# Kernel tuning notes

Hardware: AMD Instinct MI355X
Metric: run time of the kernel (lower is better)

Reference implementation:

```python
import jax, jax.numpy as jnp
import numpy as np

N_AGENTS = 5
RNN = 128
ATT = 64
N_ACT = 10
IN_DIM = 256
SIZE = 65535  # multiple of N_AGENTS -> padding branch never taken
TAU = 0.01


def _gru_cell(x, h, w_ih, w_hh, b_ih, b_hh):
    # PyTorch GRUCell math
    gi = x @ w_ih.T + b_ih
    gh = h @ w_hh.T + b_hh
    i_r, i_z, i_n = jnp.split(gi, 3, axis=-1)
    h_r, h_z, h_n = jnp.split(gh, 3, axis=-1)
    r = jax.nn.sigmoid(i_r + h_r)
    z = jax.nn.sigmoid(i_z + h_z)
    n = jnp.tanh(i_n + r * h_n)
    return (1.0 - z) * n + z * h


def _gru_seq(xs, w_ih, w_hh, b_ih, b_hh):
    # xs: [T, B, D]; zero initial hidden, returns all step outputs [T, B, RNN]
    h0 = jnp.zeros((xs.shape[1], RNN), xs.dtype)
    def step(h, x):
        h2 = _gru_cell(x, h, w_ih, w_hh, b_ih, b_hh)
        return h2, h2
    _, ys = jax.lax.scan(step, h0, xs)
    return ys


def setup_inputs():
    key = jax.random.key(0)
    ks = jax.random.split(key, 26)
    def u(k, shape, fan):
        return jax.random.uniform(k, shape, jnp.float32, -1.0, 1.0) / np.sqrt(fan)
    return {
        'obs': jax.random.normal(ks[0], (SIZE, IN_DIM), jnp.float32),
        'hidden_state': jax.random.normal(ks[1], (SIZE, RNN), jnp.float32),
        'enc_w': u(ks[2], (RNN, IN_DIM), IN_DIM), 'enc_b': u(ks[3], (RNN,), IN_DIM),
        'gru_w_ih': u(ks[4], (3 * RNN, RNN), RNN), 'gru_w_hh': u(ks[5], (3 * RNN, RNN), RNN),
        'gru_b_ih': u(ks[6], (3 * RNN,), RNN), 'gru_b_hh': u(ks[7], (3 * RNN,), RNN),
        'bi_w_ih_f': u(ks[8], (3 * RNN, 2 * RNN), RNN), 'bi_w_hh_f': u(ks[9], (3 * RNN, RNN), RNN),
        'bi_b_ih_f': u(ks[10], (3 * RNN,), RNN), 'bi_b_hh_f': u(ks[11], (3 * RNN,), RNN),
        'bi_w_ih_r': u(ks[12], (3 * RNN, 2 * RNN), RNN), 'bi_w_hh_r': u(ks[13], (3 * RNN, RNN), RNN),
        'bi_b_ih_r': u(ks[14], (3 * RNN,), RNN), 'bi_b_hh_r': u(ks[15], (3 * RNN,), RNN),
        'hard_w': u(ks[16], (2, 2 * RNN), 2 * RNN), 'hard_b': u(ks[17], (2,), 2 * RNN),
        'q_w': u(ks[18], (ATT, RNN), RNN),
        'k_w': u(ks[19], (ATT, RNN), RNN),
        'v_w': u(ks[20], (ATT, RNN), RNN), 'v_b': u(ks[21], (ATT,), RNN),
        'dec_w': u(ks[22], (N_ACT, RNN + ATT), RNN + ATT), 'dec_b': u(ks[23], (N_ACT,), RNN + ATT),
    }


def reference(obs, hidden_state, enc_w, enc_b, gru_w_ih, gru_w_hh, gru_b_ih, gru_b_hh,
              bi_w_ih_f, bi_w_hh_f, bi_b_ih_f, bi_b_hh_f,
              bi_w_ih_r, bi_w_hh_r, bi_b_ih_r, bi_b_hh_r,
              hard_w, hard_b, q_w, k_w, v_w, v_b, dec_w, dec_b):
    size = obs.shape[0]
    bpa = size // N_AGENTS  # batch per agent; SIZE is a multiple of N_AGENTS

    x = jax.nn.relu(obs @ enc_w.T + enc_b)
    h_out = _gru_cell(x, hidden_state, gru_w_ih, gru_w_hh, gru_b_ih, gru_b_hh)

    # --- hard attention: pairwise agent features -> bi-GRU -> gumbel-softmax gate ---
    # (computed exactly as in the original; note the original soft_attention
    #  ignores hard_weights, so this does not influence the returned output)
    h = h_out.reshape(bpa, N_AGENTS, RNN)
    nbr = np.array([[j for j in range(N_AGENTS) if j != i] for i in range(N_AGENTS)])  # [n, n-1]
    h_i = jnp.broadcast_to(h[:, :, None, :], (bpa, N_AGENTS, N_AGENTS - 1, RNN))
    h_j = h[:, nbr, :]                              # [bpa, n, n-1, RNN]
    pair = jnp.concatenate([h_i, h_j], axis=-1)     # [bpa, n, n-1, 2*RNN]
    seq = pair.transpose(2, 0, 1, 3).reshape(N_AGENTS - 1, bpa * N_AGENTS, 2 * RNN)
    fwd = _gru_seq(seq, bi_w_ih_f, bi_w_hh_f, bi_b_ih_f, bi_b_hh_f)
    bwd = _gru_seq(seq[::-1], bi_w_ih_r, bi_w_hh_r, bi_b_ih_r, bi_b_hh_r)[::-1]
    h_hard = jnp.concatenate([fwd, bwd], axis=-1)   # [n-1, B, 2*RNN]
    h_hard = h_hard.transpose(1, 0, 2).reshape(-1, 2 * RNN)
    logits = h_hard @ hard_w.T + hard_b             # [B*(n-1), 2]
    u01 = jax.random.uniform(jax.random.key(42), logits.shape, jnp.float32, 1e-10, 1.0)
    gumbel = -jnp.log(-jnp.log(u01))
    gs = jax.nn.softmax((logits + gumbel) / TAU, axis=-1)
    hard_weights = gs[:, 1].reshape(bpa, N_AGENTS, 1, N_AGENTS - 1).transpose(1, 0, 2, 3)
    _ = hard_weights  # unused downstream, matching the original module

    # --- soft attention: original loops per sample doing a 1x1 matmul+softmax;
    #     vectorized here. softmax over a single element is identically 1. ---
    q = h_out @ q_w.T
    k = h_out @ k_w.T
    v = jax.nn.relu(h_out @ v_w.T + v_b)
    score = jnp.sum(q * k, axis=-1, keepdims=True) / np.sqrt(ATT)  # [B,1]
    soft_w = jax.nn.softmax(score, axis=-1)                         # all ones
    x_att = v * soft_w

    final_input = jnp.concatenate([h_out, x_att], axis=-1)
    output = final_input @ dec_w.T + dec_b
    return output, h_out
```

## Files before the change

### kernel.cpp

```cpp
#include <hip/hip_runtime.h>
#include <stdint.h>

#define SIZE 65535

typedef __bf16 bf16x8 __attribute__((ext_vector_type(8)));
typedef float floatx4 __attribute__((ext_vector_type(4)));

#define WS_ENCW 0
#define WS_WIH  32768
#define WS_WHH  81920
#define WS_VW   131072
#define WS_DECW 139264
#define WS_TOTC 17792

__device__ __forceinline__ unsigned short f2bf(float f) {
    union { float f; unsigned int u; } v; v.f = f;
    unsigned int u = v.u;
    return (unsigned short)((u + 0x7fffu + ((u >> 16) & 1u)) >> 16);
}
__device__ __forceinline__ float bf2f(unsigned short b) {
    union { unsigned int u; float f; } v; v.u = ((unsigned int)b) << 16;
    return v.f;
}
__device__ __forceinline__ float sigmf(float x) {
    x = fminf(fmaxf(x, -30.f), 30.f);
    return 1.f / (1.f + __expf(-x));
}
__device__ __forceinline__ float tanhfast(float x) {
    x = fminf(fmaxf(x, -15.f), 15.f);
    float e = __expf(2.f * x);
    return (e - 1.f) / (e + 1.f);
}

union BF8 { bf16x8 v; unsigned short s[8]; };

__device__ __forceinline__ bf16x8 cvt8g(const float* p) {
    float4 a = *reinterpret_cast<const float4*>(p);
    float4 b = *reinterpret_cast<const float4*>(p + 4);
    BF8 r;
    r.s[0] = f2bf(a.x); r.s[1] = f2bf(a.y); r.s[2] = f2bf(a.z); r.s[3] = f2bf(a.w);
    r.s[4] = f2bf(b.x); r.s[5] = f2bf(b.y); r.s[6] = f2bf(b.z); r.s[7] = f2bf(b.w);
    return r.v;
}
__device__ __forceinline__ bf16x8 ld8(const unsigned short* p) {
    return *reinterpret_cast<const bf16x8*>(p);
}

__global__ __launch_bounds__(256) void cvt_weights(
    const float* __restrict__ enc_w, const float* __restrict__ w_ih,
    const float* __restrict__ w_hh, const float* __restrict__ v_w,
    const float* __restrict__ dec_w, unsigned short* __restrict__ ws) {
    int c = blockIdx.x * 256 + threadIdx.x;
    if (c >= WS_TOTC) return;
    const int lane = c & 63;
    const int l = lane & 15;
    const int q = lane >> 4;
    const float* src; int row, col, stride; bool zero = false;
    if (c < 4096) {
        int lt = c >> 6; int nt = lt >> 3, kt = lt & 7;
        row = nt * 16 + l; col = kt * 32 + q * 8; src = enc_w; stride = 256;
    } else if (c < 10240) {
        int lt = (c - 4096) >> 6; int nt = lt / 12; int r2 = lt % 12;
        int g = r2 >> 2, kt = r2 & 3;
        row = g * 128 + nt * 16 + l; col = kt * 32 + q * 8; src = w_ih; stride = 128;
    } else if (c < 16384) {
        int lt = (c - 10240) >> 6; int nt = lt / 12; int r2 = lt % 12;
        int g = r2 >> 2, kt = r2 & 3;
        row = g * 128 + nt * 16 + l; col = kt * 32 + q * 8; src = w_hh; stride = 128;
    } else if (c < 17408) {
        int lt = (c - 16384) >> 6; int nt = lt >> 2, kt = lt & 3;
        row = nt * 16 + l; col = kt * 32 + q * 8; src = v_w; stride = 128;
    } else {
        int kt = (c - 17408) >> 6;
        row = l; col = kt * 32 + q * 8; src = dec_w; stride = 192;
        zero = (l >= 10);
    }
    float4 a, b;
    if (zero) { a = make_float4(0.f,0.f,0.f,0.f); b = a; }
    else {
        const float* p = src + (size_t)row * stride + col;
        a = *reinterpret_cast<const float4*>(p);
        b = *reinterpret_cast<const float4*>(p + 4);
    }
    unsigned short* d = ws + (size_t)c * 8;
    d[0]=f2bf(a.x); d[1]=f2bf(a.y); d[2]=f2bf(a.z); d[3]=f2bf(a.w);
    d[4]=f2bf(b.x); d[5]=f2bf(b.y); d[6]=f2bf(b.z); d[7]=f2bf(b.w);
}

__global__ __launch_bounds__(256, 4) void attn_critic_kernel(
    const float* __restrict__ obs,
    const float* __restrict__ hid,
    const float* __restrict__ enc_b,
    const float* __restrict__ b_ih,
    const float* __restrict__ b_hh,
    const float* __restrict__ v_b,
    const float* __restrict__ dec_b,
    const unsigned short* __restrict__ wsw,
    float* __restrict__ out)
{
    __shared__ __align__(16) unsigned short sA[4][16][136];
    __shared__ __align__(16) unsigned short sV[4][16][72];
    __shared__ __align__(16) float sO[4][16][10];

    const int tid  = threadIdx.x;
    const int wave = tid >> 6;
    const int lane = tid & 63;
    const int l15  = lane & 15;
    const int quad = lane >> 4;
    const int wrow0 = (blockIdx.x * 4 + wave) * 16;

    int rA0 = wrow0 + l15; rA0 = (rA0 < SIZE) ? rA0 : (SIZE - 1);

    bf16x8 aob[8], hf[4];
    {
        const float* o0 = obs + (size_t)rA0 * 256;
#pragma unroll
        for (int kt = 0; kt < 8; ++kt)
            aob[kt] = cvt8g(o0 + kt * 32 + quad * 8);
        const float* h0 = hid + (size_t)rA0 * 128;
#pragma unroll
        for (int kt = 0; kt < 4; ++kt)
            hf[kt] = cvt8g(h0 + kt * 32 + quad * 8);
    }
    __builtin_amdgcn_sched_barrier(0);

    {
        const unsigned short* encf = wsw + WS_ENCW + lane * 8;
#pragma unroll 2
        for (int nt = 0; nt < 8; ++nt) {
            floatx4 a0 = floatx4{0.f,0.f,0.f,0.f};
#pragma unroll
            for (int kt = 0; kt < 8; ++kt) {
                bf16x8 b = ld8(encf + (size_t)(nt * 8 + kt) * 512);
                a0 = __builtin_amdgcn_mfma_f32_16x16x32_bf16(aob[kt], b, a0, 0, 0, 0);
            }
            float bias = enc_b[nt * 16 + l15];
#pragma unroll
            for (int r = 0; r < 4; ++r)
                sA[wave][quad * 4 + r][nt * 16 + l15] = f2bf(fmaxf(a0[r] + bias, 0.f));
        }
    }
    bf16x8 xf[4];
#pragma unroll
    for (int kt = 0; kt < 4; ++kt)
        xf[kt] = ld8(&sA[wave][l15][kt * 32 + quad * 8]);

    {
        const unsigned short* wihf = wsw + WS_WIH + lane * 8;
        const unsigned short* whhf = wsw + WS_WHH + lane * 8;
#pragma unroll 1
        for (int nt = 0; nt < 8; ++nt) {
            const int nr = nt * 16 + l15;
            floatx4 gi[3], gh[3];
#pragma unroll
            for (int g = 0; g < 3; ++g) {
                gi[g] = floatx4{0.f,0.f,0.f,0.f};
                gh[g] = gi[g];
            }
#pragma unroll
            for (int g = 0; g < 3; ++g)
#pragma unroll
                for (int kt = 0; kt < 4; ++kt) {
                    bf16x8 bi = ld8(wihf + (size_t)((nt * 3 + g) * 4 + kt) * 512);
                    bf16x8 bh = ld8(whhf + (size_t)((nt * 3 + g) * 4 + kt) * 512);
                    gi[g] = __builtin_amdgcn_mfma_f32_16x16x32_bf16(xf[kt], bi, gi[g], 0, 0, 0);
                    gh[g] = __builtin_amdgcn_mfma_f32_16x16x32_bf16(hf[kt], bh, gh[g], 0, 0, 0);
                }
            const float bir_ = b_ih[nr], biz_ = b_ih[nr + 128], bin_ = b_ih[nr + 256];
            const float bhr_ = b_hh[nr], bhz_ = b_hh[nr + 128], bhn_ = b_hh[nr + 256];
#pragma unroll
            for (int r = 0; r < 4; ++r) {
                const int grow = wrow0 + quad * 4 + r;
                const int rowc = (grow < SIZE) ? grow : (SIZE - 1);
                float hprev = hid[(size_t)rowc * 128 + nr];
                float rg = sigmf(gi[0][r] + bir_ + gh[0][r] + bhr_);
                float zg = sigmf(gi[1][r] + biz_ + gh[1][r] + bhz_);
                float ng = tanhfast(gi[2][r] + bin_ + rg * (gh[2][r] + bhn_));
                float ho = (1.f - zg) * ng + zg * hprev;
                sA[wave][quad * 4 + r][nr] = f2bf(ho);
            }
        }
    }

    {
        float* out_h = out + (size_t)SIZE * 10;
#pragma unroll 1
        for (int it = 0; it < 8; ++it) {
            int idx = it * 256 + lane * 4;
            int rr = idx >> 7, cc = idx & 127;
            int grow = wrow0 + rr;
            if (grow < SIZE) {
                float2 p0 = make_float2(bf2f(sA[wave][rr][cc]),     bf2f(sA[wave][rr][cc + 1]));
                float2 p1 = make_float2(bf2f(sA[wave][rr][cc + 2]), bf2f(sA[wave][rr][cc + 3]));
                float* dst = out_h + (size_t)grow * 128 + cc;
                *reinterpret_cast<float2*>(dst)     = p0;
                *reinterpret_cast<float2*>(dst + 2) = p1;
            }
        }
    }

    bf16x8 af[4];
#pragma unroll
    for (int kt = 0; kt < 4; ++kt)
        af[kt] = ld8(&sA[wave][l15][kt * 32 + quad * 8]);
    {
        const unsigned short* vwf = wsw + WS_VW + lane * 8;
#pragma unroll 1
        for (int nt = 0; nt < 4; ++nt) {
            floatx4 a0 = floatx4{0.f,0.f,0.f,0.f};
#pragma unroll
            for (int kt = 0; kt < 4; ++kt) {
                bf16x8 b = ld8(vwf + (size_t)(nt * 4 + kt) * 512);
                a0 = __builtin_amdgcn_mfma_f32_16x16x32_bf16(af[kt], b, a0, 0, 0, 0);
            }
            float bias = v_b[nt * 16 + l15];
#pragma unroll
            for (int r = 0; r < 4; ++r)
                sV[wave][quad * 4 + r][nt * 16 + l15] = f2bf(fmaxf(a0[r] + bias, 0.f));
        }
    }

    {
        const unsigned short* decf = wsw + WS_DECW + lane * 8;
        floatx4 d0 = floatx4{0.f,0.f,0.f,0.f};
#pragma unroll
        for (int kt = 0; kt < 6; ++kt) {
            bf16x8 b = ld8(decf + (size_t)kt * 512);
            bf16x8 a0 = (kt < 4) ? af[kt] : ld8(&sV[wave][l15][(kt - 4) * 32 + quad * 8]);
            d0 = __builtin_amdgcn_mfma_f32_16x16x32_bf16(a0, b, d0, 0, 0, 0);
        }
        if (l15 < 10) {
            float bias = dec_b[l15];
#pragma unroll
            for (int r = 0; r < 4; ++r)
                sO[wave][quad * 4 + r][l15] = d0[r] + bias;
        }
#pragma unroll
        for (int j = 0; j < 3; ++j) {
            int idx = j * 64 + lane;
            if (idx < 160) {
                int row = idx / 10, col = idx % 10;
                int grow = wrow0 + row;
                if (grow < SIZE)
                    out[(size_t)grow * 10 + col] = sO[wave][row][col];
            }
        }
    }
}

extern "C" void kernel_launch(void* const* d_in, const int* in_sizes, int n_in,
                              void* d_out, int out_size, void* d_ws, size_t ws_size,
                              hipStream_t stream) {
    const float* obs   = (const float*)d_in[0];
    const float* hid   = (const float*)d_in[1];
    const float* enc_w = (const float*)d_in[2];
    const float* enc_b = (const float*)d_in[3];
    const float* w_ih  = (const float*)d_in[4];
    const float* w_hh  = (const float*)d_in[5];
    const float* b_ih  = (const float*)d_in[6];
    const float* b_hh  = (const float*)d_in[7];
    const float* v_w   = (const float*)d_in[20];
    const float* v_b   = (const float*)d_in[21];
    const float* dec_w = (const float*)d_in[22];
    const float* dec_b = (const float*)d_in[23];
    unsigned short* wsw = (unsigned short*)d_ws;
    float* out = (float*)d_out;

    hipLaunchKernelGGL(cvt_weights, dim3((WS_TOTC + 255) / 256), dim3(256), 0, stream,
                       enc_w, w_ih, w_hh, v_w, dec_w, wsw);
    hipLaunchKernelGGL(attn_critic_kernel, dim3(1024), dim3(256), 0, stream,
                       obs, hid, enc_b, b_ih, b_hh, v_b, dec_b, wsw, out);
}
```

Before: 223.6 us.

## Stage weight fragments into shared LDS with double-buffered async global_load_lds

Previously each of the four waves in a block fetched the encoder, GRU, value and decoder weight fragments from global memory (L2) on its own. Now the block cooperatively copies each weight tile into a double-buffered LDS region with global_load_lds, prefetching the next tile while the current one feeds the MFMAs. The per-wave scratch buffers are merged into one aliased pool, float-to-bf16 conversion uses the native cast, and the hidden-state loads are hoisted ahead of the GRU MFMAs. This cuts repeated L2 weight traffic, at the price of many block-wide barriers and some lost independence between waves.

```diff
diff --git a/kernel.cpp b/kernel.cpp
--- a/kernel.cpp
+++ b/kernel.cpp
@@ -18,6 +18,10 @@
     unsigned int u = v.u;
     return (unsigned short)((u + 0x7fffu + ((u >> 16) & 1u)) >> 16);
 }
+__device__ __forceinline__ unsigned short f2bfn(float f) {
+    union { __bf16 h; unsigned short s; } u; u.h = (__bf16)f;
+    return u.s;
+}
 __device__ __forceinline__ float bf2f(unsigned short b) {
     union { unsigned int u; float f; } v; v.u = ((unsigned int)b) << 16;
     return v.f;
@@ -32,18 +36,34 @@
     return (e - 1.f) / (e + 1.f);
 }
 
-union BF8 { bf16x8 v; unsigned short s[8]; };
-
 __device__ __forceinline__ bf16x8 cvt8g(const float* p) {
     float4 a = *reinterpret_cast<const float4*>(p);
     float4 b = *reinterpret_cast<const float4*>(p + 4);
-    BF8 r;
-    r.s[0] = f2bf(a.x); r.s[1] = f2bf(a.y); r.s[2] = f2bf(a.z); r.s[3] = f2bf(a.w);
-    r.s[4] = f2bf(b.x); r.s[5] = f2bf(b.y); r.s[6] = f2bf(b.z); r.s[7] = f2bf(b.w);
-    return r.v;
+    bf16x8 r;
+    r[0] = (__bf16)a.x; r[1] = (__bf16)a.y; r[2] = (__bf16)a.z; r[3] = (__bf16)a.w;
+    r[4] = (__bf16)b.x; r[5] = (__bf16)b.y; r[6] = (__bf16)b.z; r[7] = (__bf16)b.w;
+    return r;
 }
 __device__ __forceinline__ bf16x8 ld8(const unsigned short* p) {
     return *reinterpret_cast<const bf16x8*>(p);
+}
+
+__device__ __forceinline__ void glds16(const unsigned short* g, unsigned short* l) {
+    __builtin_amdgcn_global_load_lds(
+        (const __attribute__((address_space(1))) unsigned int*)g,
+        (__attribute__((address_space(3))) unsigned int*)l, 16, 0, 0);
+}
+
+__device__ __forceinline__ void stage_seq(unsigned short* dst, const unsigned short* src,
+                                          int nfrags, int wave, int lane) {
+    for (int s = wave; s < nfrags; s += 4)
+        glds16(src + s * 512 + lane * 8, dst + s * 512);
+}
+__device__ __forceinline__ void stage_gru(unsigned short* dst, const unsigned short* wsw,
+                                          int ng, int wave, int lane) {
+    const int fo = (ng * 4 + wave) * 512 + lane * 8;
+    glds16(wsw + WS_WIH + fo, dst + wave * 512);
+    glds16(wsw + WS_WHH + fo, dst + (4 + wave) * 512);
 }
 
 __global__ __launch_bounds__(256) void cvt_weights(
@@ -98,9 +118,8 @@
     const unsigned short* __restrict__ wsw,
     float* __restrict__ out)
 {
-    __shared__ __align__(16) unsigned short sA[4][16][136];
-    __shared__ __align__(16) unsigned short sV[4][16][72];
-    __shared__ __align__(16) float sO[4][16][10];
+    __shared__ __align__(16) unsigned short wbuf[2][4096];
+    __shared__ __align__(16) unsigned short pool[4][2176];
 
     const int tid  = threadIdx.x;
     const int wave = tid >> 6;
@@ -109,7 +128,13 @@
     const int quad = lane >> 4;
     const int wrow0 = (blockIdx.x * 4 + wave) * 16;
 
+    unsigned short (*sA)[136] = (unsigned short(*)[136])&pool[wave][0];
+    unsigned short (*sV)[72]  = (unsigned short(*)[72]) &pool[wave][0];
+    float* sO = (float*)&pool[wave][1152];
+
     int rA0 = wrow0 + l15; rA0 = (rA0 < SIZE) ? rA0 : (SIZE - 1);
+
+    stage_seq(wbuf[0], wsw + WS_ENCW, 8, wave, lane);
 
     bf16x8 aob[8], hf[4];
     {
@@ -123,65 +148,78 @@
             hf[kt] = cvt8g(h0 + kt * 32 + quad * 8);
     }
     __builtin_amdgcn_sched_barrier(0);
-
-    {
-        const unsigned short* encf = wsw + WS_ENCW + lane * 8;
-#pragma unroll 2
-        for (int nt = 0; nt < 8; ++nt) {
-            floatx4 a0 = floatx4{0.f,0.f,0.f,0.f};
-#pragma unroll
-            for (int kt = 0; kt < 8; ++kt) {
-                bf16x8 b = ld8(encf + (size_t)(nt * 8 + kt) * 512);
-                a0 = __builtin_amdgcn_mfma_f32_16x16x32_bf16(aob[kt], b, a0, 0, 0, 0);
+    __syncthreads();
+
+#pragma unroll 1
+    for (int nt = 0; nt < 8; ++nt) {
+        const int cur = nt & 1;
+        if (nt < 7) stage_seq(wbuf[cur ^ 1], wsw + WS_ENCW + (nt + 1) * 4096, 8, wave, lane);
+        else        stage_gru(wbuf[cur ^ 1], wsw, 0, wave, lane);
+        const float bias = enc_b[nt * 16 + l15];
+        floatx4 a0 = floatx4{0.f,0.f,0.f,0.f};
+#pragma unroll
+        for (int kt = 0; kt < 8; ++kt) {
+            bf16x8 b = ld8(&wbuf[cur][kt * 512 + lane * 8]);
+            a0 = __builtin_amdgcn_mfma_f32_16x16x32_bf16(aob[kt], b, a0, 0, 0, 0);
+        }
+#pragma unroll
+        for (int r = 0; r < 4; ++r)
+            sA[quad * 4 + r][nt * 16 + l15] = f2bfn(fmaxf(a0[r] + bias, 0.f));
+        __syncthreads();
+    }
+
+    bf16x8 xf[4];
+#pragma unroll
+    for (int kt = 0; kt < 4; ++kt)
+        xf[kt] = ld8(&sA[l15][kt * 32 + quad * 8]);
+
+#pragma unroll 1
+    for (int nt = 0; nt < 8; ++nt) {
+        const int nr = nt * 16 + l15;
+        float hp[4];
+#pragma unroll
+        for (int r = 0; r < 4; ++r) {
+            const int grow = wrow0 + quad * 4 + r;
+            const int rowc = (grow < SIZE) ? grow : (SIZE - 1);
+            hp[r] = hid[(size_t)rowc * 128 + nr];
+        }
+        const float bir_ = b_ih[nr], biz_ = b_ih[nr + 128], bin_ = b_ih[nr + 256];
+        const float bhr_ = b_hh[nr], bhz_ = b_hh[nr + 128], bhn_ = b_hh[nr + 256];
+        floatx4 gi[3], gh[3];
+#pragma unroll
+        for (int g = 0; g < 3; ++g) {
+            gi[g] = floatx4{0.f,0.f,0.f,0.f};
+            gh[g] = gi[g];
+        }
+#pragma unroll
+        for (int g = 0; g < 3; ++g) {
+            const int cur = (nt + g) & 1;
+            const int ng = nt * 3 + g + 1;
+            if (ng < 24) stage_gru(wbuf[cur ^ 1], wsw, ng, wave, lane);
+            else         stage_seq(wbuf[cur ^ 1], wsw + WS_VW, 4, wave, lane);
+#pragma unroll
+            for (int kt = 0; kt < 4; ++kt) {
+                bf16x8 bi = ld8(&wbuf[cur][kt * 512 + lane * 8]);
+                bf16x8 bh = ld8(&wbuf[cur][(4 + kt) * 512 + lane * 8]);
+                gi[g] = __builtin_amdgcn_mfma_f32_16x16x32_bf16(xf[kt], bi, gi[g], 0, 0, 0);
+                gh[g] = __builtin_amdgcn_mfma_f32_16x16x32_bf16(hf[kt], bh, gh[g], 0, 0, 0);
             }
-            float bias = enc_b[nt * 16 + l15];
-#pragma unroll
-            for (int r = 0; r < 4; ++r)
-                sA[wave][quad * 4 + r][nt * 16 + l15] = f2bf(fmaxf(a0[r] + bias, 0.f));
-        }
-    }
-    bf16x8 xf[4];
+            __syncthreads();
+        }
+#pragma unroll
+        for (int r = 0; r < 4; ++r) {
+            float rg = sigmf(gi[0][r] + bir_ + gh[0][r] + bhr_);
+            float zg = sigmf(gi[1][r] + biz_ + gh[1][r] + bhz_);
+            float ng2 = tanhfast(gi[2][r] + bin_ + rg * (gh[2][r] + bhn_));
+            float ho = (1.f - zg) * ng2 + zg * hp[r];
+            sA[quad * 4 + r][nr] = f2bfn(ho);
+        }
+    }
+
+    bf16x8 af[4];
 #pragma unroll
     for (int kt = 0; kt < 4; ++kt)
-        xf[kt] = ld8(&sA[wave][l15][kt * 32 + quad * 8]);
-
-    {
-        const unsigned short* wihf = wsw + WS_WIH + lane * 8;
-        const unsigned short* whhf = wsw + WS_WHH + lane * 8;
-#pragma unroll 1
-        for (int nt = 0; nt < 8; ++nt) {
-            const int nr = nt * 16 + l15;
-            floatx4 gi[3], gh[3];
-#pragma unroll
-            for (int g = 0; g < 3; ++g) {
-                gi[g] = floatx4{0.f,0.f,0.f,0.f};
-                gh[g] = gi[g];
-            }
-#pragma unroll
-            for (int g = 0; g < 3; ++g)
-#pragma unroll
-                for (int kt = 0; kt < 4; ++kt) {
-                    bf16x8 bi = ld8(wihf + (size_t)((nt * 3 + g) * 4 + kt) * 512);
-                    bf16x8 bh = ld8(whhf + (size_t)((nt * 3 + g) * 4 + kt) * 512);
-                    gi[g] = __builtin_amdgcn_mfma_f32_16x16x32_bf16(xf[kt], bi, gi[g], 0, 0, 0);
-                    gh[g] = __builtin_amdgcn_mfma_f32_16x16x32_bf16(hf[kt], bh, gh[g], 0, 0, 0);
-                }
-            const float bir_ = b_ih[nr], biz_ = b_ih[nr + 128], bin_ = b_ih[nr + 256];
-            const float bhr_ = b_hh[nr], bhz_ = b_hh[nr + 128], bhn_ = b_hh[nr + 256];
-#pragma unroll
-            for (int r = 0; r < 4; ++r) {
-                const int grow = wrow0 + quad * 4 + r;
-                const int rowc = (grow < SIZE) ? grow : (SIZE - 1);
-                float hprev = hid[(size_t)rowc * 128 + nr];
-                float rg = sigmf(gi[0][r] + bir_ + gh[0][r] + bhr_);
-                float zg = sigmf(gi[1][r] + biz_ + gh[1][r] + bhz_);
-                float ng = tanhfast(gi[2][r] + bin_ + rg * (gh[2][r] + bhn_));
-                float ho = (1.f - zg) * ng + zg * hprev;
-                sA[wave][quad * 4 + r][nr] = f2bf(ho);
-            }
-        }
-    }
-
+        af[kt] = ld8(&sA[l15][kt * 32 + quad * 8]);
     {
         float* out_h = out + (size_t)SIZE * 10;
 #pragma unroll 1
@@ -190,8 +228,8 @@
             int rr = idx >> 7, cc = idx & 127;
             int grow = wrow0 + rr;
             if (grow < SIZE) {
-                float2 p0 = make_float2(bf2f(sA[wave][rr][cc]),     bf2f(sA[wave][rr][cc + 1]));
-                float2 p1 = make_float2(bf2f(sA[wave][rr][cc + 2]), bf2f(sA[wave][rr][cc + 3]));
+                float2 p0 = make_float2(bf2f(sA[rr][cc]),     bf2f(sA[rr][cc + 1]));
+                float2 p1 = make_float2(bf2f(sA[rr][cc + 2]), bf2f(sA[rr][cc + 3]));
                 float* dst = out_h + (size_t)grow * 128 + cc;
                 *reinterpret_cast<float2*>(dst)     = p0;
                 *reinterpret_cast<float2*>(dst + 2) = p1;
@@ -199,41 +237,37 @@
         }
     }
 
-    bf16x8 af[4];
-#pragma unroll
-    for (int kt = 0; kt < 4; ++kt)
-        af[kt] = ld8(&sA[wave][l15][kt * 32 + quad * 8]);
+#pragma unroll 1
+    for (int nt = 0; nt < 4; ++nt) {
+        const int cur = nt & 1;
+        if (nt < 3) stage_seq(wbuf[cur ^ 1], wsw + WS_VW + (nt + 1) * 2048, 4, wave, lane);
+        else        stage_seq(wbuf[cur ^ 1], wsw + WS_DECW, 6, wave, lane);
+        const float bias = v_b[nt * 16 + l15];
+        floatx4 a0 = floatx4{0.f,0.f,0.f,0.f};
+#pragma unroll
+        for (int kt = 0; kt < 4; ++kt) {
+            bf16x8 b = ld8(&wbuf[cur][kt * 512 + lane * 8]);
+            a0 = __builtin_amdgcn_mfma_f32_16x16x32_bf16(af[kt], b, a0, 0, 0, 0);
+        }
+#pragma unroll
+        for (int r = 0; r < 4; ++r)
+            sV[quad * 4 + r][nt * 16 + l15] = f2bfn(fmaxf(a0[r] + bias, 0.f));
+        __syncthreads();
+    }
+
     {
-        const unsigned short* vwf = wsw + WS_VW + lane * 8;
-#pragma unroll 1
-        for (int nt = 0; nt < 4; ++nt) {
-            floatx4 a0 = floatx4{0.f,0.f,0.f,0.f};
-#pragma unroll
-            for (int kt = 0; kt < 4; ++kt) {
-                bf16x8 b = ld8(vwf + (size_t)(nt * 4 + kt) * 512);
-                a0 = __builtin_amdgcn_mfma_f32_16x16x32_bf16(af[kt], b, a0, 0, 0, 0);
-            }
-            float bias = v_b[nt * 16 + l15];
+        floatx4 d0 = floatx4{0.f,0.f,0.f,0.f};
+#pragma unroll
+        for (int kt = 0; kt < 6; ++kt) {
+            bf16x8 b = ld8(&wbuf[0][kt * 512 + lane * 8]);
+            bf16x8 a0 = (kt < 4) ? af[kt] : ld8(&sV[l15][(kt - 4) * 32 + quad * 8]);
+            d0 = __builtin_amdgcn_mfma_f32_16x16x32_bf16(a0, b, d0, 0, 0, 0);
+        }
+        if (l15 < 10) {
+            const float bias = dec_b[l15];
 #pragma unroll
             for (int r = 0; r < 4; ++r)
-                sV[wave][quad * 4 + r][nt * 16 + l15] = f2bf(fmaxf(a0[r] + bias, 0.f));
-        }
-    }
-
-    {
-        const unsigned short* decf = wsw + WS_DECW + lane * 8;
-        floatx4 d0 = floatx4{0.f,0.f,0.f,0.f};
-#pragma unroll
-        for (int kt = 0; kt < 6; ++kt) {
-            bf16x8 b = ld8(decf + (size_t)kt * 512);
-            bf16x8 a0 = (kt < 4) ? af[kt] : ld8(&sV[wave][l15][(kt - 4) * 32 + quad * 8]);
-            d0 = __builtin_amdgcn_mfma_f32_16x16x32_bf16(a0, b, d0, 0, 0, 0);
-        }
-        if (l15 < 10) {
-            float bias = dec_b[l15];
-#pragma unroll
-            for (int r = 0; r < 4; ++r)
-                sO[wave][quad * 4 + r][l15] = d0[r] + bias;
+                sO[(quad * 4 + r) * 10 + l15] = d0[r] + bias;
         }
 #pragma unroll
         for (int j = 0; j < 3; ++j) {
@@ -242,7 +276,7 @@
                 int row = idx / 10, col = idx % 10;
                 int grow = wrow0 + row;
                 if (grow < SIZE)
-                    out[(size_t)grow * 10 + col] = sO[wave][row][col];
+                    out[(size_t)grow * 10 + col] = sO[row * 10 + col];
             }
         }
     }
```

Measured after the change: 208.5 us. 1.07x faster.
